# Kernel tuning notes

Measured on AMD Instinct MI355X. Metric: run time of the kernel, lower is better.

## Reference

```python
import jax, jax.numpy as jnp
import numpy as np

D = 64            # number of devices (leaves hold D/8 each)
B = 65536         # batch of states
FEAT = 5 + 4 * D  # 261
HID = 128


def setup_inputs() -> dict:
    key = jax.random.key(0)
    ks = jax.random.split(key, 10)
    def nrm(k, shape, s=0.1):
        return jax.random.normal(k, shape, jnp.float32) * s
    return {
        "x": jax.random.normal(ks[0], (B, FEAT), jnp.float32),
        # gate params per depth d: 2^d nodes, weight dim 5 + 4*D/2^d
        "w0": nrm(ks[1], (1, 5 + 4 * D)),
        "b0": jnp.zeros((1,), jnp.float32),
        "w1": nrm(ks[2], (2, 5 + 4 * (D // 2))),
        "b1": jnp.zeros((2,), jnp.float32),
        "w2": nrm(ks[3], (4, 5 + 4 * (D // 4))),
        "b2": jnp.zeros((4,), jnp.float32),
        # leaf prob_dist (torch inits to zeros; random here for a non-trivial baseline)
        "leaf_probs": nrm(ks[4], (8, D // 8), 1.0),
        # critic MLP
        "Wc1": nrm(ks[5], (FEAT, HID)),
        "bc1": jnp.zeros((HID,), jnp.float32),
        "Wc2": nrm(ks[6], (HID, 1)),
        "bc2": jnp.zeros((1,), jnp.float32),
    }


def reference(x, w0, b0, w1, b1, w2, b2, leaf_probs, Wc1, bc1, Wc2, bc2):
    # Batched deterministic ClusterTree routing (exploration disabled).
    x5 = x[:, :5]                       # (B, 5) global features
    dev = x[:, 5:].reshape(B, D, 4)     # (B, D, 4) per-device features
    node = jnp.zeros((B,), jnp.int32)   # current node index at each depth
    cum = jnp.ones((B,), x.dtype)       # product of gate values along path
    for d, (wd, bd) in enumerate([(w0, b0), (w1, b1), (w2, b2)]):
        nd = D >> d                     # devices per node at this depth
        off = node * nd                 # contiguous-cluster start offset
        idx = off[:, None] + jnp.arange(nd)                     # (B, nd)
        dslice = jnp.take_along_axis(dev, idx[:, :, None], 1)   # (B, nd, 4)
        w = wd[node]                    # (B, 5 + 4*nd)
        gate = (jnp.sum(x5 * w[:, :5], -1)
                + jnp.sum(dslice.reshape(B, -1) * w[:, 5:], -1)
                + bd[node])
        val = jax.nn.sigmoid(gate)
        cum = cum * val                 # torch: val * child_output, recursively
        node = node * 2 + (val >= 0.5).astype(jnp.int32)
    p = cum[:, None] * leaf_probs[node]                 # (B, D//8)
    v = jax.nn.relu(x @ Wc1 + bc1) @ Wc2 + bc2          # (B, 1) critic
    return p, v
```

## Files before the change

kernel.cpp:

```cpp
#include <hip/hip_runtime.h>
#include <hip/hip_bf16.h>
#include <stdint.h>

#define NB    65536
#define FEATN 261
#define HIDN  128
#define NSTEP 17
#define SROW  296

#define ROWSF 64
#define NTHRF 256

typedef __attribute__((ext_vector_type(8)))  short bf16x8;
typedef __attribute__((ext_vector_type(16))) float f32x16;
typedef float f32x4u __attribute__((ext_vector_type(4), aligned(4)));

#define MFMA32(A, B, C) __builtin_amdgcn_mfma_f32_32x32x16_bf16(A, B, C, 0, 0, 0)

__device__ __forceinline__ uint16_t f2b(float v) {
    __hip_bfloat16 b = __float2bfloat16(v);
    return *reinterpret_cast<uint16_t*>(&b);
}

__device__ __forceinline__ float sigmoidf(float g) {
    return 1.f / (1.f + __expf(-g));
}

#define RED16(v) do { v += __shfl_xor(v, 1); v += __shfl_xor(v, 2); \
                      v += __shfl_xor(v, 4); v += __shfl_xor(v, 8); } while (0)

__global__ void prep_kernel(const float* __restrict__ Wc1,
                            uint16_t* __restrict__ wsB)
{
    int t = blockIdx.x * 256 + threadIdx.x;
    if (t < NSTEP * 4 * 64) {
        int p = t >> 6, l = t & 63;
        int s = p >> 2, nt = p & 3;
        int n = nt * 32 + (l & 31);
        int kb = 16 * s + 8 * (l >> 5);
        uint16_t hw[8];
        #pragma unroll
        for (int j = 0; j < 8; ++j) {
            int k = kb + j;
            float v = (k < FEATN) ? Wc1[(size_t)k * HIDN + n] : 0.f;
            hw[j] = f2b(v);
        }
        *reinterpret_cast<uint4*>(wsB + (size_t)p * 512 + l * 8) =
            *reinterpret_cast<uint4*>(hw);
    }
}

__global__ __launch_bounds__(NTHRF, 4) void fused_kernel(
    const float* __restrict__ x,
    const float* __restrict__ w0, const float* __restrict__ b0,
    const float* __restrict__ w1, const float* __restrict__ b1,
    const float* __restrict__ w2, const float* __restrict__ b2,
    const float* __restrict__ leaf,
    const uint16_t* __restrict__ wsB,
    const float* __restrict__ bc1, const float* __restrict__ Wc2,
    const float* __restrict__ bc2,
    float* __restrict__ out_p, float* __restrict__ out_v)
{
    __shared__ uint16_t Axs[ROWSF * SROW];
    __shared__ float bc1s[HIDN];
    __shared__ float wc2s[HIDN];
    __shared__ float vpart[ROWSF * 2];

    const int tid = threadIdx.x;
    const int rowBase = blockIdx.x * ROWSF;

    if (tid < HIDN) { bc1s[tid] = bc1[tid]; wc2s[tid] = Wc2[tid]; }
    if (tid < ROWSF) {
        uint16_t* rp = Axs + tid * SROW;
        rp[261] = 0;
        *reinterpret_cast<uint32_t*>(rp + 262) = 0u;
        uint4 z; z.x = z.y = z.z = z.w = 0u;
        *reinterpret_cast<uint4*>(rp + 264) = z;
        *reinterpret_cast<uint4*>(rp + 272) = z;
        *reinterpret_cast<uint4*>(rp + 280) = z;
        *reinterpret_cast<uint4*>(rp + 288) = z;
    }

    const int s = tid & 15;
    const int g = tid >> 4;

    f32x4u w0q[4];
    #pragma unroll
    for (int j = 0; j < 4; ++j)
        w0q[j] = *reinterpret_cast<const f32x4u*>(w0 + 64 * j + 4 * s);
    const float w0t = (s < 5) ? w0[256 + s] : 0.f;

    float w1v[4][4], w2v[4][4];
    #pragma unroll
    for (int j = 0; j < 4; ++j)
        #pragma unroll
        for (int c = 0; c < 4; ++c) {
            int e = 64 * j + 4 * s + c;
            w1v[j][c] = w1[(e < 133) ? e : e + 5];
            int n2 = (e < 5) ? 0 : ((e - 5) >> 6);
            w2v[j][c] = w2[e + 5 * n2];
        }
    const float w1t = (s < 5) ? w1[261 + s] : 0.f;
    const float w2t = (s < 5) ? w2[271 + s] : 0.f;

    const float xw1b  = (s < 5) ? w1[133 + s] : 0.f;
    const float xw2_1 = (s < 5) ? w2[ 69 + s] : 0.f;
    const float xw2_2 = (s < 5) ? w2[138 + s] : 0.f;
    const float xw2_3 = (s < 5) ? w2[207 + s] : 0.f;

    const float b0s  = b0[0];
    const float b1s0 = b1[0], b1s1 = b1[1];
    const float b2s0 = b2[0], b2s1 = b2[1], b2s2 = b2[2], b2s3 = b2[3];

    #pragma unroll 1
    for (int r4 = 0; r4 < 4; ++r4) {
        const int rl  = r4 * 16 + g;
        const int row = rowBase + rl;
        const float* xr = x + (size_t)row * FEATN;

        f32x4u xq[4];
        #pragma unroll
        for (int j = 0; j < 4; ++j)
            xq[j] = *reinterpret_cast<const f32x4u*>(xr + 64 * j + 4 * s);
        const float xt  = (s < 5) ? xr[256 + s] : 0.f;
        const float xs5 = (s < 5) ? xr[s]       : 0.f;

        {
            uint16_t* rp = Axs + rl * SROW;
            #pragma unroll
            for (int j = 0; j < 4; ++j) {
                uint32_t p0w = (uint32_t)f2b(xq[j][0]) | ((uint32_t)f2b(xq[j][1]) << 16);
                uint32_t p1w = (uint32_t)f2b(xq[j][2]) | ((uint32_t)f2b(xq[j][3]) << 16);
                uint2 pk; pk.x = p0w; pk.y = p1w;
                *reinterpret_cast<uint2*>(rp + 64 * j + 4 * s) = pk;
            }
            if (s < 5) rp[256 + s] = f2b(xt);
        }

        float p0 = 0.f, p1a = 0.f, p1b = 0.f;
        float p2_0 = 0.f, p2_1 = 0.f, p2_2 = 0.f, p2_3 = 0.f;
        #pragma unroll
        for (int j = 0; j < 4; ++j)
            #pragma unroll
            for (int c = 0; c < 4; ++c) {
                const float xv = xq[j][c];
                const bool lo = (4 * s + c) < 5;
                p0 += xv * w0q[j][c];
                const float t1 = xv * w1v[j][c];
                const float t2 = xv * w2v[j][c];
                if (j == 0) {
                    p1a += t1;
                    p2_0 += t2;
                } else if (j == 1) {
                    p1a += t1;
                    p2_0 += lo ? t2 : 0.f;  p2_1 += lo ? 0.f : t2;
                } else if (j == 2) {
                    p1a += lo ? t1 : 0.f;   p1b += lo ? 0.f : t1;
                    p2_1 += lo ? t2 : 0.f;  p2_2 += lo ? 0.f : t2;
                } else {
                    p1b += t1;
                    p2_2 += lo ? t2 : 0.f;  p2_3 += lo ? 0.f : t2;
                }
            }
        p0   += xt * w0t;
        p1b  += xt * w1t;
        p2_3 += xt * w2t;
        p1b  += xs5 * xw1b;
        p2_1 += xs5 * xw2_1;
        p2_2 += xs5 * xw2_2;
        p2_3 += xs5 * xw2_3;

        RED16(p0);
        const float gate0 = p0 + b0s;
        int nn = (gate0 >= 0.f) ? 1 : 0;
        float cum = sigmoidf(gate0);

        float p1 = nn ? p1b : p1a;
        RED16(p1);
        const float gate1 = p1 + (nn ? b1s1 : b1s0);
        nn = nn * 2 + ((gate1 >= 0.f) ? 1 : 0);
        cum *= sigmoidf(gate1);

        float p2 = (nn & 2) ? ((nn & 1) ? p2_3 : p2_2)
                            : ((nn & 1) ? p2_1 : p2_0);
        RED16(p2);
        const float gate2 = p2 + ((nn & 2) ? ((nn & 1) ? b2s3 : b2s2)
                                           : ((nn & 1) ? b2s1 : b2s0));
        nn = nn * 2 + ((gate2 >= 0.f) ? 1 : 0);
        cum *= sigmoidf(gate2);

        if (s < 8)
            out_p[(size_t)row * 8 + s] = cum * leaf[nn * 8 + s];
    }

    __syncthreads();

    const int lane = tid & 63;
    const int w    = tid >> 6;
    const int mt   = w >> 1;
    const int nh   = w & 1;

    const uint16_t* arow = Axs + (mt * 32 + (lane & 31)) * SROW + (lane >> 5) * 8;
    const uint16_t* bgl  = wsB + (size_t)(2 * nh) * 512 + lane * 8;

    f32x16 acc0 = {}, acc1 = {};
    #pragma unroll
    for (int ss = 0; ss < NSTEP; ++ss) {
        bf16x8 af  = *reinterpret_cast<const bf16x8*>(arow + ss * 16);
        bf16x8 bf0 = *reinterpret_cast<const bf16x8*>(bgl + (size_t)(ss * 4)     * 512);
        bf16x8 bf1 = *reinterpret_cast<const bf16x8*>(bgl + (size_t)(ss * 4 + 1) * 512);
        acc0 = MFMA32(af, bf0, acc0);
        acc1 = MFMA32(af, bf1, acc1);
    }

    {
        const int c = lane & 31;
        const int q = lane >> 5;
        const int n0 = 2 * nh * 32 + c;
        const int n1 = n0 + 32;
        const float bb0 = bc1s[n0], ww0 = wc2s[n0];
        const float bb1 = bc1s[n1], ww1 = wc2s[n1];

        float pv[16];
        #pragma unroll
        for (int reg = 0; reg < 16; ++reg) {
            float h0 = acc0[reg] + bb0; h0 = h0 > 0.f ? h0 : 0.f;
            float h1 = acc1[reg] + bb1; h1 = h1 > 0.f ? h1 : 0.f;
            float t = h0 * ww0 + h1 * ww1;
            t += __shfl_xor(t, 1);
            t += __shfl_xor(t, 2);
            t += __shfl_xor(t, 4);
            t += __shfl_xor(t, 8);
            t += __shfl_xor(t, 16);
            pv[reg] = t;
        }
        #pragma unroll
        for (int reg = 0; reg < 16; ++reg) {
            if (c == reg) {
                int row_local = (reg & 3) + 8 * (reg >> 2) + 4 * q;
                vpart[(mt * 32 + row_local) * 2 + nh] = pv[reg];
            }
        }
    }
    __syncthreads();
    if (tid < ROWSF)
        out_v[rowBase + tid] = vpart[tid * 2] + vpart[tid * 2 + 1] + bc2[0];
}

extern "C" void kernel_launch(void* const* d_in, const int* in_sizes, int n_in,
                              void* d_out, int out_size, void* d_ws, size_t ws_size,
                              hipStream_t stream) {
    const float* x    = (const float*)d_in[0];
    const float* w0   = (const float*)d_in[1];
    const float* b0   = (const float*)d_in[2];
    const float* w1   = (const float*)d_in[3];
    const float* b1   = (const float*)d_in[4];
    const float* w2   = (const float*)d_in[5];
    const float* b2   = (const float*)d_in[6];
    const float* leaf = (const float*)d_in[7];
    const float* Wc1  = (const float*)d_in[8];
    const float* bc1  = (const float*)d_in[9];
    const float* Wc2  = (const float*)d_in[10];
    const float* bc2  = (const float*)d_in[11];

    uint16_t* wsB = (uint16_t*)d_ws;

    float* out_p = (float*)d_out;
    float* out_v = out_p + (size_t)NB * 8;

    prep_kernel<<<17, 256, 0, stream>>>(Wc1, wsB);
    fused_kernel<<<NB / ROWSF, NTHRF, 0, stream>>>(
        x, w0, b0, w1, b1, w2, b2, leaf, wsB, bc1, Wc2, bc2, out_p, out_v);
}
```

Measured before the change: 128.0 us.

## Double block threads to 512 and split critic MFMA across four wave N-tiles

Raises the block size from 256 to 512 threads, so each 16-lane group now handles 2 rows instead of 4. Both rows' x loads are issued up front before any compute, giving more memory-level parallelism. In the critic GEMM each wave now owns one 32-column N tile instead of two, and the partial value sums are reduced over four slots. This spreads the memory-bound load phase over more waves, at the cost of larger blocks that may lower how many blocks fit per CU under the launch bound of 4.

```diff
diff --git a/kernel.cpp b/kernel.cpp
--- a/kernel.cpp
+++ b/kernel.cpp
@@ -9,7 +9,7 @@
 #define SROW  296
 
 #define ROWSF 64
-#define NTHRF 256
+#define NTHRF 512
 
 typedef __attribute__((ext_vector_type(8)))  short bf16x8;
 typedef __attribute__((ext_vector_type(16))) float f32x16;
@@ -64,7 +64,7 @@
     __shared__ uint16_t Axs[ROWSF * SROW];
     __shared__ float bc1s[HIDN];
     __shared__ float wc2s[HIDN];
-    __shared__ float vpart[ROWSF * 2];
+    __shared__ float vpart[ROWSF * 4];
 
     const int tid = threadIdx.x;
     const int rowBase = blockIdx.x * ROWSF;
@@ -112,30 +112,34 @@
     const float b1s0 = b1[0], b1s1 = b1[1];
     const float b2s0 = b2[0], b2s1 = b2[1], b2s2 = b2[2], b2s3 = b2[3];
 
-    #pragma unroll 1
-    for (int r4 = 0; r4 < 4; ++r4) {
-        const int rl  = r4 * 16 + g;
-        const int row = rowBase + rl;
-        const float* xr = x + (size_t)row * FEATN;
-
-        f32x4u xq[4];
+    f32x4u xq[2][4];
+    float xt[2], xs5[2];
+    #pragma unroll
+    for (int r2 = 0; r2 < 2; ++r2) {
+        const float* xr = x + (size_t)(rowBase + r2 * 32 + g) * FEATN;
         #pragma unroll
         for (int j = 0; j < 4; ++j)
-            xq[j] = *reinterpret_cast<const f32x4u*>(xr + 64 * j + 4 * s);
-        const float xt  = (s < 5) ? xr[256 + s] : 0.f;
-        const float xs5 = (s < 5) ? xr[s]       : 0.f;
-
-        {
-            uint16_t* rp = Axs + rl * SROW;
-            #pragma unroll
-            for (int j = 0; j < 4; ++j) {
-                uint32_t p0w = (uint32_t)f2b(xq[j][0]) | ((uint32_t)f2b(xq[j][1]) << 16);
-                uint32_t p1w = (uint32_t)f2b(xq[j][2]) | ((uint32_t)f2b(xq[j][3]) << 16);
-                uint2 pk; pk.x = p0w; pk.y = p1w;
-                *reinterpret_cast<uint2*>(rp + 64 * j + 4 * s) = pk;
-            }
-            if (s < 5) rp[256 + s] = f2b(xt);
-        }
+            xq[r2][j] = *reinterpret_cast<const f32x4u*>(xr + 64 * j + 4 * s);
+        xt[r2]  = (s < 5) ? xr[256 + s] : 0.f;
+        xs5[r2] = (s < 5) ? xr[s]       : 0.f;
+    }
+
+    #pragma unroll
+    for (int r2 = 0; r2 < 2; ++r2) {
+        uint16_t* rp = Axs + (r2 * 32 + g) * SROW;
+        #pragma unroll
+        for (int j = 0; j < 4; ++j) {
+            uint32_t p0w = (uint32_t)f2b(xq[r2][j][0]) | ((uint32_t)f2b(xq[r2][j][1]) << 16);
+            uint32_t p1w = (uint32_t)f2b(xq[r2][j][2]) | ((uint32_t)f2b(xq[r2][j][3]) << 16);
+            uint2 pk; pk.x = p0w; pk.y = p1w;
+            *reinterpret_cast<uint2*>(rp + 64 * j + 4 * s) = pk;
+        }
+        if (s < 5) rp[256 + s] = f2b(xt[r2]);
+    }
+
+    #pragma unroll
+    for (int r2 = 0; r2 < 2; ++r2) {
+        const int row = rowBase + r2 * 32 + g;
 
         float p0 = 0.f, p1a = 0.f, p1b = 0.f;
         float p2_0 = 0.f, p2_1 = 0.f, p2_2 = 0.f, p2_3 = 0.f;
@@ -143,7 +147,7 @@
         for (int j = 0; j < 4; ++j)
             #pragma unroll
             for (int c = 0; c < 4; ++c) {
-                const float xv = xq[j][c];
+                const float xv = xq[r2][j][c];
                 const bool lo = (4 * s + c) < 5;
                 p0 += xv * w0q[j][c];
                 const float t1 = xv * w1v[j][c];
@@ -162,13 +166,13 @@
                     p2_2 += lo ? t2 : 0.f;  p2_3 += lo ? 0.f : t2;
                 }
             }
-        p0   += xt * w0t;
-        p1b  += xt * w1t;
-        p2_3 += xt * w2t;
-        p1b  += xs5 * xw1b;
-        p2_1 += xs5 * xw2_1;
-        p2_2 += xs5 * xw2_2;
-        p2_3 += xs5 * xw2_3;
+        p0   += xt[r2] * w0t;
+        p1b  += xt[r2] * w1t;
+        p2_3 += xt[r2] * w2t;
+        p1b  += xs5[r2] * xw1b;
+        p2_1 += xs5[r2] * xw2_1;
+        p2_2 += xs5[r2] * xw2_2;
+        p2_3 += xs5[r2] * xw2_3;
 
         RED16(p0);
         const float gate0 = p0 + b0s;
@@ -197,36 +201,31 @@
 
     const int lane = tid & 63;
     const int w    = tid >> 6;
-    const int mt   = w >> 1;
-    const int nh   = w & 1;
+    const int mt   = w >> 2;
+    const int nt   = w & 3;
 
     const uint16_t* arow = Axs + (mt * 32 + (lane & 31)) * SROW + (lane >> 5) * 8;
-    const uint16_t* bgl  = wsB + (size_t)(2 * nh) * 512 + lane * 8;
-
-    f32x16 acc0 = {}, acc1 = {};
+    const uint16_t* bgl  = wsB + (size_t)nt * 512 + lane * 8;
+
+    f32x16 acc = {};
     #pragma unroll
     for (int ss = 0; ss < NSTEP; ++ss) {
-        bf16x8 af  = *reinterpret_cast<const bf16x8*>(arow + ss * 16);
-        bf16x8 bf0 = *reinterpret_cast<const bf16x8*>(bgl + (size_t)(ss * 4)     * 512);
-        bf16x8 bf1 = *reinterpret_cast<const bf16x8*>(bgl + (size_t)(ss * 4 + 1) * 512);
-        acc0 = MFMA32(af, bf0, acc0);
-        acc1 = MFMA32(af, bf1, acc1);
+        bf16x8 af = *reinterpret_cast<const bf16x8*>(arow + ss * 16);
+        bf16x8 bf = *reinterpret_cast<const bf16x8*>(bgl + (size_t)(ss * 4) * 512);
+        acc = MFMA32(af, bf, acc);
     }
 
     {
         const int c = lane & 31;
         const int q = lane >> 5;
-        const int n0 = 2 * nh * 32 + c;
-        const int n1 = n0 + 32;
-        const float bb0 = bc1s[n0], ww0 = wc2s[n0];
-        const float bb1 = bc1s[n1], ww1 = wc2s[n1];
+        const int n = nt * 32 + c;
+        const float bb = bc1s[n], ww = wc2s[n];
 
         float pv[16];
         #pragma unroll
         for (int reg = 0; reg < 16; ++reg) {
-            float h0 = acc0[reg] + bb0; h0 = h0 > 0.f ? h0 : 0.f;
-            float h1 = acc1[reg] + bb1; h1 = h1 > 0.f ? h1 : 0.f;
-            float t = h0 * ww0 + h1 * ww1;
+            float h = acc[reg] + bb; h = h > 0.f ? h : 0.f;
+            float t = h * ww;
             t += __shfl_xor(t, 1);
             t += __shfl_xor(t, 2);
             t += __shfl_xor(t, 4);
@@ -238,13 +237,14 @@
         for (int reg = 0; reg < 16; ++reg) {
             if (c == reg) {
                 int row_local = (reg & 3) + 8 * (reg >> 2) + 4 * q;
-                vpart[(mt * 32 + row_local) * 2 + nh] = pv[reg];
+                vpart[(mt * 32 + row_local) * 4 + nt] = pv[reg];
             }
         }
     }
     __syncthreads();
     if (tid < ROWSF)
-        out_v[rowBase + tid] = vpart[tid * 2] + vpart[tid * 2 + 1] + bc2[0];
+        out_v[rowBase + tid] = (vpart[tid * 4] + vpart[tid * 4 + 1])
+                             + (vpart[tid * 4 + 2] + vpart[tid * 4 + 3]) + bc2[0];
 }
 
 extern "C" void kernel_launch(void* const* d_in, const int* in_sizes, int n_in,
```

Result: slower. 134.5 us (+5.1%).

## Halve rows per block and split MFMA N across four waves

Applied to the files above, without the earlier changes.

Each block now handles 32 rows instead of 64, and the four waves each compute one 32-column slice of the critic hidden layer with a single accumulator instead of two. The LDS row stride shrinks, and launch bounds now request 8 blocks per CU. The goal is higher occupancy and more blocks to hide global-load latency on the memory-bound x read. The cost is that each wave reloads the shared Wc1 B-fragments for fewer rows, so per-block weight traffic is amortized over half as many rows. The launch code likely needs a doubled grid, and it is not shown.

```diff
diff --git a/kernel.cpp b/kernel.cpp
--- a/kernel.cpp
+++ b/kernel.cpp
@@ -6,9 +6,9 @@
 #define FEATN 261
 #define HIDN  128
 #define NSTEP 17
-#define SROW  296
-
-#define ROWSF 64
+#define SROW  280
+
+#define ROWSF 32
 #define NTHRF 256
 
 typedef __attribute__((ext_vector_type(8)))  short bf16x8;
@@ -50,7 +50,7 @@
     }
 }
 
-__global__ __launch_bounds__(NTHRF, 4) void fused_kernel(
+__global__ __launch_bounds__(NTHRF, 8) void fused_kernel(
     const float* __restrict__ x,
     const float* __restrict__ w0, const float* __restrict__ b0,
     const float* __restrict__ w1, const float* __restrict__ b1,
@@ -64,7 +64,7 @@
     __shared__ uint16_t Axs[ROWSF * SROW];
     __shared__ float bc1s[HIDN];
     __shared__ float wc2s[HIDN];
-    __shared__ float vpart[ROWSF * 2];
+    __shared__ float vpart[ROWSF * 4];
 
     const int tid = threadIdx.x;
     const int rowBase = blockIdx.x * ROWSF;
@@ -77,8 +77,6 @@
         uint4 z; z.x = z.y = z.z = z.w = 0u;
         *reinterpret_cast<uint4*>(rp + 264) = z;
         *reinterpret_cast<uint4*>(rp + 272) = z;
-        *reinterpret_cast<uint4*>(rp + 280) = z;
-        *reinterpret_cast<uint4*>(rp + 288) = z;
     }
 
     const int s = tid & 15;
@@ -113,8 +111,8 @@
     const float b2s0 = b2[0], b2s1 = b2[1], b2s2 = b2[2], b2s3 = b2[3];
 
     #pragma unroll 1
-    for (int r4 = 0; r4 < 4; ++r4) {
-        const int rl  = r4 * 16 + g;
+    for (int r2 = 0; r2 < 2; ++r2) {
+        const int rl  = r2 * 16 + g;
         const int row = rowBase + rl;
         const float* xr = x + (size_t)row * FEATN;
 
@@ -197,36 +195,29 @@
 
     const int lane = tid & 63;
     const int w    = tid >> 6;
-    const int mt   = w >> 1;
-    const int nh   = w & 1;
-
-    const uint16_t* arow = Axs + (mt * 32 + (lane & 31)) * SROW + (lane >> 5) * 8;
-    const uint16_t* bgl  = wsB + (size_t)(2 * nh) * 512 + lane * 8;
-
-    f32x16 acc0 = {}, acc1 = {};
+
+    const uint16_t* arow = Axs + (size_t)(lane & 31) * SROW + (lane >> 5) * 8;
+    const uint16_t* bgl  = wsB + (size_t)w * 512 + lane * 8;
+
+    f32x16 acc = {};
     #pragma unroll
     for (int ss = 0; ss < NSTEP; ++ss) {
-        bf16x8 af  = *reinterpret_cast<const bf16x8*>(arow + ss * 16);
-        bf16x8 bf0 = *reinterpret_cast<const bf16x8*>(bgl + (size_t)(ss * 4)     * 512);
-        bf16x8 bf1 = *reinterpret_cast<const bf16x8*>(bgl + (size_t)(ss * 4 + 1) * 512);
-        acc0 = MFMA32(af, bf0, acc0);
-        acc1 = MFMA32(af, bf1, acc1);
+        bf16x8 af = *reinterpret_cast<const bf16x8*>(arow + ss * 16);
+        bf16x8 bf = *reinterpret_cast<const bf16x8*>(bgl + (size_t)(ss * 4) * 512);
+        acc = MFMA32(af, bf, acc);
     }
 
     {
         const int c = lane & 31;
         const int q = lane >> 5;
-        const int n0 = 2 * nh * 32 + c;
-        const int n1 = n0 + 32;
-        const float bb0 = bc1s[n0], ww0 = wc2s[n0];
-        const float bb1 = bc1s[n1], ww1 = wc2s[n1];
+        const int n = w * 32 + c;
+        const float bb = bc1s[n], ww = wc2s[n];
 
         float pv[16];
         #pragma unroll
         for (int reg = 0; reg < 16; ++reg) {
-            float h0 = acc0[reg] + bb0; h0 = h0 > 0.f ? h0 : 0.f;
-            float h1 = acc1[reg] + bb1; h1 = h1 > 0.f ? h1 : 0.f;
-            float t = h0 * ww0 + h1 * ww1;
+            float h = acc[reg] + bb; h = h > 0.f ? h : 0.f;
+            float t = h * ww;
             t += __shfl_xor(t, 1);
             t += __shfl_xor(t, 2);
             t += __shfl_xor(t, 4);
@@ -238,13 +229,14 @@
         for (int reg = 0; reg < 16; ++reg) {
             if (c == reg) {
                 int row_local = (reg & 3) + 8 * (reg >> 2) + 4 * q;
-                vpart[(mt * 32 + row_local) * 2 + nh] = pv[reg];
+                vpart[row_local * 4 + w] = pv[reg];
             }
         }
     }
     __syncthreads();
     if (tid < ROWSF)
-        out_v[rowBase + tid] = vpart[tid * 2] + vpart[tid * 2 + 1] + bc2[0];
+        out_v[rowBase + tid] = (vpart[tid * 4] + vpart[tid * 4 + 1])
+                             + (vpart[tid * 4 + 2] + vpart[tid * 4 + 3]) + bc2[0];
 }
 
 extern "C" void kernel_launch(void* const* d_in, const int* in_sizes, int n_in,
```

Measured after the change: 183.1 us. 1.43x slower.
